# Kernel optimization log

Measured on AMD Instinct MI355X. Metric: run time of the kernel, lower is better.

The kernel has to match this reference:

```python
import jax, jax.numpy as jnp
import numpy as np
import math

NUM_HEADS = 8
D_HEAD = 128
DEPTH = 1
LAMBDA_INIT = 0.8 - 0.6 * math.exp(-0.3 * DEPTH)
EPS = 1e-5


def setup_inputs() -> dict:
    key = jax.random.key(0)
    ks = jax.random.split(key, 10)
    B, N, D = 2, 2048, 1024
    s = 0.02
    return {
        "X": jax.random.normal(ks[0], (B, N, D), jnp.float32),
        "Wq": jax.random.normal(ks[1], (2 * D_HEAD * NUM_HEADS, D), jnp.float32) * s,
        "Wk": jax.random.normal(ks[2], (2 * D_HEAD * NUM_HEADS, D), jnp.float32) * s,
        "Wv": jax.random.normal(ks[3], (2 * D_HEAD * NUM_HEADS, D), jnp.float32) * s,
        "Wo": jax.random.normal(ks[4], (D, 2 * D_HEAD * NUM_HEADS), jnp.float32) * s,
        "lambda_q1": jax.random.normal(ks[5], (NUM_HEADS, D_HEAD), jnp.float32) * 0.1,
        "lambda_k1": jax.random.normal(ks[6], (NUM_HEADS, D_HEAD), jnp.float32) * 0.1,
        "lambda_q2": jax.random.normal(ks[7], (NUM_HEADS, D_HEAD), jnp.float32) * 0.1,
        "lambda_k2": jax.random.normal(ks[8], (NUM_HEADS, D_HEAD), jnp.float32) * 0.1,
        "rms_scale": jnp.ones((2 * D_HEAD,), jnp.float32),
    }


def reference(X, Wq, Wk, Wv, Wo, lambda_q1, lambda_k1, lambda_q2, lambda_k2, rms_scale):
    B, N, D = X.shape
    H, dh = NUM_HEADS, D_HEAD

    def proj(W):
        # (B, N, 2*H*dh) -> (B, H, N, 2*dh)
        y = jnp.einsum('bnd,ed->bne', X, W)
        return y.reshape(B, N, H, 2 * dh).transpose(0, 2, 1, 3)

    Q = proj(Wq)
    K = proj(Wk)
    V = proj(Wv)
    Q1, Q2 = Q[..., :dh], Q[..., dh:]
    K1, K2 = K[..., :dh], K[..., dh:]

    lam1 = jnp.exp(jnp.sum(lambda_q1 * lambda_k1, axis=-1))  # (H,)
    lam2 = jnp.exp(jnp.sum(lambda_q2 * lambda_k2, axis=-1))
    lam = (lam1 - lam2 + LAMBDA_INIT)[None, :, None, None]  # (1, H, 1, 1)

    scaling = 1.0 / math.sqrt(dh)
    A1 = jnp.einsum('bhqd,bhkd->bhqk', Q1, K1) * scaling
    A2 = jnp.einsum('bhqd,bhkd->bhqk', Q2, K2) * scaling
    attn = jax.nn.softmax(A1, axis=-1) - lam * jax.nn.softmax(A2, axis=-1)

    O = jnp.einsum('bhqk,bhkd->bhqd', attn, V)  # (B, H, N, 2*dh)
    rms = jnp.sqrt(jnp.mean(O * O, axis=-1, keepdims=True) + EPS)
    O = O / rms * rms_scale
    O = O * (1.0 - LAMBDA_INIT)
    O = O.transpose(0, 2, 1, 3).reshape(B, N, H * 2 * dh)
    return jnp.einsum('bne,de->bnd', O, Wo)
```

## Files before the change

kernel.cpp:

```cpp
#include <hip/hip_runtime.h>
#include <hip/hip_bf16.h>

typedef __bf16 bf16;
typedef __attribute__((ext_vector_type(8))) __bf16 bf16x8;
typedef __attribute__((ext_vector_type(4))) float f32x4;

#define LAMBDA_INIT_F 0.3555090675909693f
#define RMS_EPS 1e-5f
#define QSCALE_F 0.1275174053237f

__device__ __forceinline__ void gl_lds16(const bf16* g, bf16* l) {
  __builtin_amdgcn_global_load_lds(
      (const __attribute__((address_space(1))) unsigned int*)g,
      (__attribute__((address_space(3))) unsigned int*)l, 16, 0, 0);
}

__global__ void fused_cast(const float* __restrict__ X, const float* __restrict__ Wq,
                           const float* __restrict__ Wk, const float* __restrict__ Wv,
                           const float* __restrict__ Wo, const float* __restrict__ rs,
                           bf16* __restrict__ out) {
  constexpr int T4 = 3145728;
  constexpr float OSC = 1.0f - LAMBDA_INIT_F;
  int idx = blockIdx.x * blockDim.x + threadIdx.x;
  int stride = gridDim.x * blockDim.x;
  for (int i = idx; i < T4; i += stride) {
    const float* src;
    int off;
    bool isWo = false;
    if (i < 1048576)       { src = X;  off = i; }
    else if (i < 1572864)  { src = Wq; off = i - 1048576; }
    else if (i < 2097152)  { src = Wk; off = i - 1572864; }
    else if (i < 2621440)  { src = Wv; off = i - 2097152; }
    else                   { src = Wo; off = i - 2621440; isWo = true; }
    float4 v = reinterpret_cast<const float4*>(src)[off];
    if (isWo) {
      int r0 = (off * 4) & 255;
      v.x *= rs[r0] * OSC; v.y *= rs[r0 + 1] * OSC;
      v.z *= rs[r0 + 2] * OSC; v.w *= rs[r0 + 3] * OSC;
    }
    bf16 o[4];
    o[0] = (bf16)v.x; o[1] = (bf16)v.y; o[2] = (bf16)v.z; o[3] = (bf16)v.w;
    *reinterpret_cast<ushort4*>(&out[(size_t)i * 4]) = *reinterpret_cast<const ushort4*>(o);
  }
}

template <int MODE, int BM>
__global__ __launch_bounds__(256) void gemm_bt(
    const bf16* __restrict__ A, const bf16* __restrict__ B,
    void* __restrict__ Cv, int M, int N, int K) {
  constexpr int BN = 128, BK = 32;
  constexpr int MF = BM / 32;
  constexpr int CA = BM / 16;
  __shared__ __align__(16) bf16 As[2][BM * BK];
  __shared__ __align__(16) bf16 Bs[2][BN * BK];
  const int tid = threadIdx.x, lane = tid & 63, w = tid >> 6;
  const int l15 = lane & 15, lhi = lane >> 4;
  const int wr = (w >> 1) * (BM / 2), wc = (w & 1) * 64;
  const int bm = blockIdx.x * BM, bn = blockIdx.y * BN;
  const int srow = lane >> 2, scol = (lane & 3) * 8;
  const int NTK = K / BK;
  f32x4 acc[MF][4] = {};

  auto stage = [&](int buf, int k0) {
#pragma unroll
    for (int i = 0; i < CA / 4; ++i) {
      int c = w * (CA / 4) + i;
      gl_lds16(&A[(size_t)(bm + c * 16 + srow) * K + k0 + scol], &As[buf][c * 512]);
    }
#pragma unroll
    for (int i = 0; i < 2; ++i) {
      int c = w * 2 + i;
      gl_lds16(&B[(size_t)(bn + c * 16 + srow) * K + k0 + scol], &Bs[buf][c * 512]);
    }
  };

  stage(0, 0);
  __syncthreads();
  for (int t = 0; t < NTK; ++t) {
    const int buf = t & 1;
    if (t + 1 < NTK) stage(buf ^ 1, (t + 1) * BK);
    bf16x8 af[MF], bfr[4];
#pragma unroll
    for (int mf = 0; mf < MF; ++mf)
      af[mf] = *reinterpret_cast<const bf16x8*>(&As[buf][(wr + mf * 16 + l15) * BK + lhi * 8]);
#pragma unroll
    for (int nf = 0; nf < 4; ++nf)
      bfr[nf] = *reinterpret_cast<const bf16x8*>(&Bs[buf][(wc + nf * 16 + l15) * BK + lhi * 8]);
#pragma unroll
    for (int mf = 0; mf < MF; ++mf)
#pragma unroll
      for (int nf = 0; nf < 4; ++nf)
        acc[mf][nf] = __builtin_amdgcn_mfma_f32_16x16x32_bf16(af[mf], bfr[nf], acc[mf][nf], 0, 0, 0);
    __syncthreads();
  }

#pragma unroll
  for (int mf = 0; mf < MF; ++mf)
#pragma unroll
    for (int nf = 0; nf < 4; ++nf)
#pragma unroll
      for (int r = 0; r < 4; ++r) {
        int m = bm + wr + mf * 16 + lhi * 4 + r;
        int n = bn + wc + nf * 16 + l15;
        if constexpr (MODE == 1) {
          ((float*)Cv)[(size_t)m * N + n] = acc[mf][nf][r];
        } else {
          int reg = n >> 11, nl = n & 2047;
          if (reg == 0) {
            ((bf16*)Cv)[(size_t)m * 2048 + nl] = (bf16)(acc[mf][nf][r] * QSCALE_F);
          } else if (reg == 1) {
            ((bf16*)Cv)[(size_t)(m + 4096) * 2048 + nl] = (bf16)acc[mf][nf][r];
          } else {
            int bb = m >> 11, nq = m & 2047;
            int hh = nl >> 8, e = nl & 255;
            int k5 = nq & 31;
            int slot = (((k5 >> 2) & 3) << 3) | (((k5 >> 4) & 1) << 2) | (k5 & 3);
            int np = (nq & ~31) | slot;
            ((bf16*)Cv)[(size_t)16777216 + ((((size_t)bb * 8 + hh) * 256 + e) << 11) + np] =
                (bf16)acc[mf][nf][r];
          }
        }
      }
}

__global__ __launch_bounds__(512, 4) void diff_attn(
    const bf16* __restrict__ Q, const bf16* __restrict__ Kb, const bf16* __restrict__ Vtg,
    const float* __restrict__ lq1, const float* __restrict__ lk1,
    const float* __restrict__ lq2, const float* __restrict__ lk2,
    bf16* __restrict__ Ob) {
  constexpr int NSEQ = 2048, E = 2048, KT = 32, NT = NSEQ / KT;
  __shared__ __align__(16) char smem[65536];
  bf16* Zb = (bf16*)smem;

  const int tid = threadIdx.x, lane = tid & 63, w = tid >> 6;
  const int l15 = lane & 15, lhi = lane >> 4;
  const int g = w >> 1, s = w & 1;

  const int bid = blockIdx.x;
  const int orig = (bid & 7) * 64 + (bid >> 3);
  const int bh = orig >> 5;
  const int qb = orig & 31;
  const int b = bh >> 3, h = bh & 7;
  const int q0 = qb * 64;

  float lam = 0.f;
  if (s) {
    float sl1 = 0.f, sl2 = 0.f;
    for (int i = 0; i < 128; ++i) {
      sl1 += lq1[h * 128 + i] * lk1[h * 128 + i];
      sl2 += lq2[h * 128 + i] * lk2[h * 128 + i];
    }
    lam = __expf(sl1) - __expf(sl2) + LAMBDA_INIT_F;
  }

  const size_t qbase = ((size_t)b * NSEQ + q0 + g * 16 + l15) * E + (size_t)h * 256 + s * 128;
  bf16x8 qf[4];
#pragma unroll
  for (int df = 0; df < 4; ++df)
    qf[df] = *reinterpret_cast<const bf16x8*>(&Q[qbase + df * 32 + lhi * 8]);

  const bf16* Kbase = Kb + ((size_t)b * NSEQ) * E + (size_t)h * 256;
  const bf16* Vbase = Vtg + (((size_t)b * 8 + h) * 256) * (size_t)NSEQ;

  const int krow_sub = lane >> 5;
  const int kslot = lane & 31;
  const int ve_sub = lane >> 2;
  const int vchunk = lane & 3;
  const int swz = l15 & 7;
  const int vq2 = (l15 >> 1) & 3;
  const int voff = (lhi ^ vq2) << 3;

  f32x4 o[16] = {};
  float ll = 0.f;

  auto stage = [&](int buf, int t) {
    const int kt0 = t * KT;
    bf16* Ksl = (bf16*)(smem + buf * 32768);
    bf16* Vsl = Ksl + 8192;
#pragma unroll
    for (int i = 0; i < 2; ++i) {
      int c = w * 2 + i;
      int row = 2 * c + krow_sub;
      gl_lds16(&Kbase[(size_t)(kt0 + row) * E + ((kslot ^ (row & 7)) << 3)], &Ksl[c * 512]);
    }
#pragma unroll
    for (int i = 0; i < 2; ++i) {
      int c = w * 2 + i;
      int e = c * 16 + ve_sub;
      int lc = vchunk ^ ((e >> 1) & 3);
      gl_lds16(&Vbase[(size_t)e * NSEQ + kt0 + (lc << 3)], &Vsl[c * 512]);
    }
  };

  stage(0, 0);
  __syncthreads();

  for (int t = 0; t < NT; ++t) {
    const int buf = t & 1;
    const bf16* Ksl = (const bf16*)(smem + buf * 32768);
    const bf16* Vsl = Ksl + 8192;

    f32x4 sv0 = {}, sv1 = {};
#pragma unroll
    for (int df = 0; df < 4; ++df) {
      const int slot = (((s << 4) + df * 4 + lhi) ^ swz) << 3;
      bf16x8 kf0 = *reinterpret_cast<const bf16x8*>(&Ksl[l15 * 256 + slot]);
      bf16x8 kf1 = *reinterpret_cast<const bf16x8*>(&Ksl[(16 + l15) * 256 + slot]);
      sv0 = __builtin_amdgcn_mfma_f32_16x16x32_bf16(kf0, qf[df], sv0, 0, 0, 0);
      sv1 = __builtin_amdgcn_mfma_f32_16x16x32_bf16(kf1, qf[df], sv1, 0, 0, 0);
    }

    __builtin_amdgcn_sched_barrier(0);
    if (t + 1 < NT) stage(buf ^ 1, t + 1);
    __builtin_amdgcn_sched_barrier(0);

    bf16 pb[8];
    float rsum = 0.f;
#pragma unroll
    for (int r = 0; r < 4; ++r) {
      float e0 = __builtin_amdgcn_exp2f(sv0[r]);
      float e1 = __builtin_amdgcn_exp2f(sv1[r]);
      rsum += e0 + e1;
      pb[r] = (bf16)e0;
      pb[4 + r] = (bf16)e1;
    }
    ll += rsum;
    bf16x8 pa = *reinterpret_cast<const bf16x8*>(pb);

    __builtin_amdgcn_s_setprio(1);
#pragma unroll
    for (int eb = 0; eb < 16; ++eb) {
      bf16x8 vf = *reinterpret_cast<const bf16x8*>(&Vsl[(eb * 16 + l15) * 32 + voff]);
      o[eb] = __builtin_amdgcn_mfma_f32_16x16x32_bf16(pa, vf, o[eb], 0, 0, 0);
    }
    __builtin_amdgcn_s_setprio(0);

    __syncthreads();
  }

  ll += __shfl_xor(ll, 16, 64);
  ll += __shfl_xor(ll, 32, 64);
  float L[4];
#pragma unroll
  for (int r = 0; r < 4; ++r) L[r] = __shfl(ll, 4 * lhi + r, 64);

  if (s) {
    bf16* Zg = Zb + g * 4096;
#pragma unroll
    for (int r = 0; r < 4; ++r) {
      float i2 = lam / L[r];
#pragma unroll
      for (int eb = 0; eb < 16; ++eb)
        Zg[(4 * lhi + r) * 256 + eb * 16 + l15] = (bf16)(o[eb][r] * i2);
    }
  }
  __syncthreads();
  if (!s) {
    const bf16* Zg = Zb + g * 4096;
#pragma unroll
    for (int r = 0; r < 4; ++r) {
      float i1 = 1.0f / L[r];
      float vals[16];
      float ssq = 0.f;
#pragma unroll
      for (int eb = 0; eb < 16; ++eb) {
        float v = o[eb][r] * i1 - (float)Zg[(4 * lhi + r) * 256 + eb * 16 + l15];
        vals[eb] = v;
        ssq += v * v;
      }
#pragma unroll
      for (int off = 1; off < 16; off <<= 1) ssq += __shfl_xor(ssq, off, 64);
      float rinv = rsqrtf(ssq * (1.0f / 256.0f) + RMS_EPS);
      const int q = q0 + g * 16 + 4 * lhi + r;
      const size_t ob = ((size_t)b * NSEQ + q) * E + (size_t)h * 256;
#pragma unroll
      for (int eb = 0; eb < 16; ++eb) {
        int e = eb * 16 + l15;
        Ob[ob + e] = (bf16)(vals[eb] * rinv);
      }
    }
  }
}

extern "C" void kernel_launch(void* const* d_in, const int* in_sizes, int n_in,
                              void* d_out, int out_size, void* d_ws, size_t ws_size,
                              hipStream_t stream) {
  const float* X   = (const float*)d_in[0];
  const float* Wq  = (const float*)d_in[1];
  const float* Wk  = (const float*)d_in[2];
  const float* Wv  = (const float*)d_in[3];
  const float* Wo  = (const float*)d_in[4];
  const float* lq1 = (const float*)d_in[5];
  const float* lk1 = (const float*)d_in[6];
  const float* lq2 = (const float*)d_in[7];
  const float* lk2 = (const float*)d_in[8];
  const float* rs  = (const float*)d_in[9];
  float* out = (float*)d_out;

  constexpr size_t B = 2, NSEQ = 2048, D = 1024, E = 2048;
  constexpr size_t M = B * NSEQ;

  char* ws = (char*)d_ws;
  bf16* Xb  = (bf16*)ws;
  bf16* Wqb = Xb + M * D;
  bf16* Wkb = Wqb + E * D;
  bf16* Wvb = Wkb + E * D;
  bf16* Wob = Wvb + E * D;
  bf16* Qb  = Wob + D * E;
  bf16* Kb  = Qb + M * E;
  bf16* Vtb = Kb + M * E;
  bf16* Ob  = Vtb + M * E;

  fused_cast<<<2048, 256, 0, stream>>>(X, Wq, Wk, Wv, Wo, rs, Xb);

  gemm_bt<3, 128><<<dim3(M / 128, 6144 / 128), 256, 0, stream>>>(
      Xb, Wqb, Qb, (int)M, 6144, (int)D);

  diff_attn<<<dim3(512), 512, 0, stream>>>(Qb, Kb, Vtb, lq1, lk1, lq2, lk2, Ob);

  gemm_bt<1, 128><<<dim3(M / 128, D / 128), 256, 0, stream>>>(Ob, Wob, out, (int)M, (int)D, (int)E);
}
```

Before: 243.5 us.

## Process two query subtiles per wave in diff attention, halving block threads

Each wave now computes scores and PV products for 32 query rows (two 16-row subtiles), so every K and V fragment read from shared memory feeds two MFMAs. The block drops to 256 threads (4 waves) with the same 64-query tile, and the K/V staging is split so two waves load K and two load V, each issuing 8 async loads. This is meant to cut LDS read traffic per MFMA. In exchange, accumulator register use roughly doubles, the launch bound allows fewer waves per SIMD, and there is less parallelism to hide latency.

```diff
diff --git a/kernel.cpp b/kernel.cpp
--- a/kernel.cpp
+++ b/kernel.cpp
@@ -123,7 +123,7 @@
       }
 }
 
-__global__ __launch_bounds__(512, 4) void diff_attn(
+__global__ __launch_bounds__(256, 2) void diff_attn(
     const bf16* __restrict__ Q, const bf16* __restrict__ Kb, const bf16* __restrict__ Vtg,
     const float* __restrict__ lq1, const float* __restrict__ lk1,
     const float* __restrict__ lq2, const float* __restrict__ lk2,
@@ -153,11 +153,13 @@
     lam = __expf(sl1) - __expf(sl2) + LAMBDA_INIT_F;
   }
 
-  const size_t qbase = ((size_t)b * NSEQ + q0 + g * 16 + l15) * E + (size_t)h * 256 + s * 128;
-  bf16x8 qf[4];
-#pragma unroll
-  for (int df = 0; df < 4; ++df)
-    qf[df] = *reinterpret_cast<const bf16x8*>(&Q[qbase + df * 32 + lhi * 8]);
+  const size_t qbase = ((size_t)b * NSEQ + q0 + g * 32 + l15) * E + (size_t)h * 256 + s * 128;
+  bf16x8 qlo[4], qhi[4];
+#pragma unroll
+  for (int df = 0; df < 4; ++df) {
+    qlo[df] = *reinterpret_cast<const bf16x8*>(&Q[qbase + df * 32 + lhi * 8]);
+    qhi[df] = *reinterpret_cast<const bf16x8*>(&Q[qbase + 16 * E + df * 32 + lhi * 8]);
+  }
 
   const bf16* Kbase = Kb + ((size_t)b * NSEQ) * E + (size_t)h * 256;
   const bf16* Vbase = Vtg + (((size_t)b * 8 + h) * 256) * (size_t)NSEQ;
@@ -170,25 +172,28 @@
   const int vq2 = (l15 >> 1) & 3;
   const int voff = (lhi ^ vq2) << 3;
 
-  f32x4 o[16] = {};
-  float ll = 0.f;
+  f32x4 olo[16] = {}, ohi[16] = {};
+  float ll0 = 0.f, ll1 = 0.f;
 
   auto stage = [&](int buf, int t) {
     const int kt0 = t * KT;
     bf16* Ksl = (bf16*)(smem + buf * 32768);
     bf16* Vsl = Ksl + 8192;
-#pragma unroll
-    for (int i = 0; i < 2; ++i) {
-      int c = w * 2 + i;
-      int row = 2 * c + krow_sub;
-      gl_lds16(&Kbase[(size_t)(kt0 + row) * E + ((kslot ^ (row & 7)) << 3)], &Ksl[c * 512]);
-    }
-#pragma unroll
-    for (int i = 0; i < 2; ++i) {
-      int c = w * 2 + i;
-      int e = c * 16 + ve_sub;
-      int lc = vchunk ^ ((e >> 1) & 3);
-      gl_lds16(&Vbase[(size_t)e * NSEQ + kt0 + (lc << 3)], &Vsl[c * 512]);
+    if (w < 2) {
+#pragma unroll
+      for (int i = 0; i < 8; ++i) {
+        int c = w * 8 + i;
+        int row = 2 * c + krow_sub;
+        gl_lds16(&Kbase[(size_t)(kt0 + row) * E + ((kslot ^ (row & 7)) << 3)], &Ksl[c * 512]);
+      }
+    } else {
+#pragma unroll
+      for (int i = 0; i < 8; ++i) {
+        int c = (w - 2) * 8 + i;
+        int e = c * 16 + ve_sub;
+        int lc = vchunk ^ ((e >> 1) & 3);
+        gl_lds16(&Vbase[(size_t)e * NSEQ + kt0 + (lc << 3)], &Vsl[c * 512]);
+      }
     }
   };
 
@@ -200,83 +205,106 @@
     const bf16* Ksl = (const bf16*)(smem + buf * 32768);
     const bf16* Vsl = Ksl + 8192;
 
-    f32x4 sv0 = {}, sv1 = {};
+    f32x4 s0l = {}, s1l = {}, s0h = {}, s1h = {};
 #pragma unroll
     for (int df = 0; df < 4; ++df) {
       const int slot = (((s << 4) + df * 4 + lhi) ^ swz) << 3;
       bf16x8 kf0 = *reinterpret_cast<const bf16x8*>(&Ksl[l15 * 256 + slot]);
       bf16x8 kf1 = *reinterpret_cast<const bf16x8*>(&Ksl[(16 + l15) * 256 + slot]);
-      sv0 = __builtin_amdgcn_mfma_f32_16x16x32_bf16(kf0, qf[df], sv0, 0, 0, 0);
-      sv1 = __builtin_amdgcn_mfma_f32_16x16x32_bf16(kf1, qf[df], sv1, 0, 0, 0);
+      s0l = __builtin_amdgcn_mfma_f32_16x16x32_bf16(kf0, qlo[df], s0l, 0, 0, 0);
+      s0h = __builtin_amdgcn_mfma_f32_16x16x32_bf16(kf0, qhi[df], s0h, 0, 0, 0);
+      s1l = __builtin_amdgcn_mfma_f32_16x16x32_bf16(kf1, qlo[df], s1l, 0, 0, 0);
+      s1h = __builtin_amdgcn_mfma_f32_16x16x32_bf16(kf1, qhi[df], s1h, 0, 0, 0);
     }
 
     __builtin_amdgcn_sched_barrier(0);
     if (t + 1 < NT) stage(buf ^ 1, t + 1);
     __builtin_amdgcn_sched_barrier(0);
 
-    bf16 pb[8];
-    float rsum = 0.f;
+    bf16 pbl[8], pbh[8];
+    float r0 = 0.f, r1 = 0.f;
 #pragma unroll
     for (int r = 0; r < 4; ++r) {
-      float e0 = __builtin_amdgcn_exp2f(sv0[r]);
-      float e1 = __builtin_amdgcn_exp2f(sv1[r]);
-      rsum += e0 + e1;
-      pb[r] = (bf16)e0;
-      pb[4 + r] = (bf16)e1;
-    }
-    ll += rsum;
-    bf16x8 pa = *reinterpret_cast<const bf16x8*>(pb);
+      float e0 = __builtin_amdgcn_exp2f(s0l[r]);
+      float e1 = __builtin_amdgcn_exp2f(s1l[r]);
+      r0 += e0 + e1;
+      pbl[r] = (bf16)e0;
+      pbl[4 + r] = (bf16)e1;
+      float e2 = __builtin_amdgcn_exp2f(s0h[r]);
+      float e3 = __builtin_amdgcn_exp2f(s1h[r]);
+      r1 += e2 + e3;
+      pbh[r] = (bf16)e2;
+      pbh[4 + r] = (bf16)e3;
+    }
+    ll0 += r0;
+    ll1 += r1;
+    bf16x8 pal = *reinterpret_cast<const bf16x8*>(pbl);
+    bf16x8 pah = *reinterpret_cast<const bf16x8*>(pbh);
 
     __builtin_amdgcn_s_setprio(1);
 #pragma unroll
     for (int eb = 0; eb < 16; ++eb) {
       bf16x8 vf = *reinterpret_cast<const bf16x8*>(&Vsl[(eb * 16 + l15) * 32 + voff]);
-      o[eb] = __builtin_amdgcn_mfma_f32_16x16x32_bf16(pa, vf, o[eb], 0, 0, 0);
+      olo[eb] = __builtin_amdgcn_mfma_f32_16x16x32_bf16(pal, vf, olo[eb], 0, 0, 0);
+      ohi[eb] = __builtin_amdgcn_mfma_f32_16x16x32_bf16(pah, vf, ohi[eb], 0, 0, 0);
     }
     __builtin_amdgcn_s_setprio(0);
 
     __syncthreads();
   }
 
-  ll += __shfl_xor(ll, 16, 64);
-  ll += __shfl_xor(ll, 32, 64);
-  float L[4];
-#pragma unroll
-  for (int r = 0; r < 4; ++r) L[r] = __shfl(ll, 4 * lhi + r, 64);
-
+  ll0 += __shfl_xor(ll0, 16, 64);
+  ll0 += __shfl_xor(ll0, 32, 64);
+  ll1 += __shfl_xor(ll1, 16, 64);
+  ll1 += __shfl_xor(ll1, 32, 64);
+  float L0[4], L1[4];
+#pragma unroll
+  for (int r = 0; r < 4; ++r) {
+    L0[r] = __shfl(ll0, 4 * lhi + r, 64);
+    L1[r] = __shfl(ll1, 4 * lhi + r, 64);
+  }
+
+  bf16* Zg = Zb + g * 8192;
   if (s) {
-    bf16* Zg = Zb + g * 4096;
 #pragma unroll
     for (int r = 0; r < 4; ++r) {
-      float i2 = lam / L[r];
-#pragma unroll
-      for (int eb = 0; eb < 16; ++eb)
-        Zg[(4 * lhi + r) * 256 + eb * 16 + l15] = (bf16)(o[eb][r] * i2);
+      float i2l = lam / L0[r];
+      float i2h = lam / L1[r];
+#pragma unroll
+      for (int eb = 0; eb < 16; ++eb) {
+        Zg[(4 * lhi + r) * 256 + eb * 16 + l15] = (bf16)(olo[eb][r] * i2l);
+        Zg[(16 + 4 * lhi + r) * 256 + eb * 16 + l15] = (bf16)(ohi[eb][r] * i2h);
+      }
     }
   }
   __syncthreads();
   if (!s) {
-    const bf16* Zg = Zb + g * 4096;
-#pragma unroll
-    for (int r = 0; r < 4; ++r) {
-      float i1 = 1.0f / L[r];
-      float vals[16];
-      float ssq = 0.f;
-#pragma unroll
-      for (int eb = 0; eb < 16; ++eb) {
-        float v = o[eb][r] * i1 - (float)Zg[(4 * lhi + r) * 256 + eb * 16 + l15];
-        vals[eb] = v;
-        ssq += v * v;
-      }
-#pragma unroll
-      for (int off = 1; off < 16; off <<= 1) ssq += __shfl_xor(ssq, off, 64);
-      float rinv = rsqrtf(ssq * (1.0f / 256.0f) + RMS_EPS);
-      const int q = q0 + g * 16 + 4 * lhi + r;
-      const size_t ob = ((size_t)b * NSEQ + q) * E + (size_t)h * 256;
-#pragma unroll
-      for (int eb = 0; eb < 16; ++eb) {
-        int e = eb * 16 + l15;
-        Ob[ob + e] = (bf16)(vals[eb] * rinv);
+#pragma unroll
+    for (int half = 0; half < 2; ++half) {
+      const f32x4* oh = half ? ohi : olo;
+      const float* Lh = half ? L1 : L0;
+#pragma unroll
+      for (int r = 0; r < 4; ++r) {
+        float i1 = 1.0f / Lh[r];
+        float vals[16];
+        float ssq = 0.f;
+#pragma unroll
+        for (int eb = 0; eb < 16; ++eb) {
+          float v = oh[eb][r] * i1 -
+                    (float)Zg[(half * 16 + 4 * lhi + r) * 256 + eb * 16 + l15];
+          vals[eb] = v;
+          ssq += v * v;
+        }
+#pragma unroll
+        for (int off = 1; off < 16; off <<= 1) ssq += __shfl_xor(ssq, off, 64);
+        float rinv = rsqrtf(ssq * (1.0f / 256.0f) + RMS_EPS);
+        const int q = q0 + g * 32 + half * 16 + 4 * lhi + r;
+        const size_t ob = ((size_t)b * NSEQ + q) * E + (size_t)h * 256;
+#pragma unroll
+        for (int eb = 0; eb < 16; ++eb) {
+          int e = eb * 16 + l15;
+          Ob[ob + e] = (bf16)(vals[eb] * rinv);
+        }
       }
     }
   }
@@ -316,7 +344,7 @@
   gemm_bt<3, 128><<<dim3(M / 128, 6144 / 128), 256, 0, stream>>>(
       Xb, Wqb, Qb, (int)M, 6144, (int)D);
 
-  diff_attn<<<dim3(512), 512, 0, stream>>>(Qb, Kb, Vtb, lq1, lk1, lq2, lk2, Ob);
+  diff_attn<<<dim3(512), 256, 0, stream>>>(Qb, Kb, Vtb, lq1, lk1, lq2, lk2, Ob);
 
   gemm_bt<1, 128><<<dim3(M / 128, D / 128), 256, 0, stream>>>(Ob, Wob, out, (int)M, (int)D, (int)E);
 }
```

Result: faster. 236.8 us (-2.7%).
